# Kernel optimization log

Hardware: AMD Instinct MI355X
Metric: run time of the kernel (lower is better)

The kernel has to match this reference:

```python
import jax, jax.numpy as jnp
import numpy as np

E = 8          # num_experts
K = 2          # num_experts_per_tok
NORM_TOPK = True
B, S, D, F = 2, 1024, 2048, 1024  # batch, seq, hidden, moe_intermediate


def _kaiming_uniform(key, shape):
    # moe_fused_kaiming_uniform_: bound = sqrt(3*5 / in_features), in_features = shape[-1]
    bound = float(np.sqrt(3.0 * 5.0 / shape[-1]))
    return jax.random.uniform(key, shape, jnp.float32, -bound, bound)


def setup_inputs() -> dict:
    key = jax.random.key(0)
    k0, k1, k2, k3, k4 = jax.random.split(key, 5)
    gate_bound = float(1.0 / np.sqrt(D))  # nn.Linear default init
    return {
        "hidden_states": jax.random.normal(k0, (B, S, D), jnp.float32),
        "gate_w": jax.random.uniform(k1, (E, D), jnp.float32, -gate_bound, gate_bound),
        "w_gate_proj": _kaiming_uniform(k2, (E, F, D)),
        "w_up_proj": _kaiming_uniform(k3, (E, F, D)),
        "w_down_proj": _kaiming_uniform(k4, (E, D, F)),
    }


def reference(hidden_states, gate_w, w_gate_proj, w_up_proj, w_down_proj):
    b, s, d = hidden_states.shape
    x = hidden_states.reshape(-1, d)                      # [T, D]
    T = x.shape[0]

    # Router: softmax in fp32, top-k, optional renorm
    router_logits = x @ gate_w.T                          # [T, E]
    probs = jax.nn.softmax(router_logits.astype(jnp.float32), axis=-1)
    routing_weights, selected = jax.lax.top_k(probs, K)   # [T, K], [T, K]
    if NORM_TOPK:
        routing_weights = routing_weights / routing_weights.sum(-1, keepdims=True)
    routing_weights = routing_weights.astype(x.dtype)

    # Dense combine weights: c[t, e] = sum_k rw[t,k] * (sel[t,k]==e)
    combine = jnp.zeros((T, E), x.dtype).at[jnp.arange(T)[:, None], selected].add(routing_weights)

    # Expert SwiGLU FFN (dense over experts; combine zeros out unrouted experts,
    # identical math to sorted grouped-GEMM dispatch in the original)
    g = jnp.einsum('td,efd->tef', x, w_gate_proj)         # [T, E, F]
    u = jnp.einsum('td,efd->tef', x, w_up_proj)           # [T, E, F]
    h = jax.nn.silu(g) * u                                # [T, E, F]
    out = jnp.einsum('tef,edf,te->td', h, w_down_proj, combine)  # [T, D]

    return out.reshape(b, s, d), router_logits
```

## Files before the change

### kernel.cpp

```cpp
#include <hip/hip_runtime.h>
#include <stdint.h>

#define T_TOK 2048
#define DIM   2048
#define FDIM  1024
#define NE    8
#define MAXTILES 40

typedef __attribute__((ext_vector_type(8))) short short8;
typedef __attribute__((ext_vector_type(4))) float f32x4;

__device__ __forceinline__ unsigned short f2b(float f) {
  union { float f; unsigned int i; } x; x.f = f;
  unsigned int r = x.i + 0x7fffu + ((x.i >> 16) & 1u);
  return (unsigned short)(r >> 16);
}

__device__ __forceinline__ void async16(void* lds, const void* g) {
  __builtin_amdgcn_global_load_lds(
      (const __attribute__((address_space(1))) void*)g,
      (__attribute__((address_space(3))) void*)lds, 16, 0, 0);
}

__global__ __launch_bounds__(256) void cvt_x_k(const float* __restrict__ x,
                                               unsigned short* __restrict__ xb)
{
  int i = (blockIdx.x * 256 + threadIdx.x) * 8;
  float4 a = *(const float4*)(x + i);
  float4 b = *(const float4*)(x + i + 4);
  ushort4 o0, o1;
  o0.x = f2b(a.x); o0.y = f2b(a.y); o0.z = f2b(a.z); o0.w = f2b(a.w);
  o1.x = f2b(b.x); o1.y = f2b(b.y); o1.z = f2b(b.z); o1.w = f2b(b.w);
  *(ushort4*)(xb + i) = o0;
  *(ushort4*)(xb + i + 4) = o1;
}

__global__ __launch_bounds__(256) void router_k(
    const float* __restrict__ x, const float* __restrict__ gw,
    float* __restrict__ topkw, int* __restrict__ topke, int* __restrict__ counts,
    float* __restrict__ logits_out)
{
  int wave = threadIdx.x >> 6, lane = threadIdx.x & 63;
  int t = blockIdx.x * 4 + wave;
  const float* xr = x + (size_t)t * DIM;
  float acc[NE];
#pragma unroll
  for (int e = 0; e < NE; e++) acc[e] = 0.f;
  for (int d = lane * 4; d < DIM; d += 256) {
    float4 xv = *(const float4*)(xr + d);
#pragma unroll
    for (int e = 0; e < NE; e++) {
      float4 gv = *(const float4*)(gw + e * DIM + d);
      acc[e] += xv.x * gv.x + xv.y * gv.y + xv.z * gv.z + xv.w * gv.w;
    }
  }
#pragma unroll
  for (int off = 32; off > 0; off >>= 1) {
#pragma unroll
    for (int e = 0; e < NE; e++) acc[e] += __shfl_down(acc[e], off);
  }
  if (lane == 0) {
    float m = acc[0];
#pragma unroll
    for (int e = 1; e < NE; e++) m = fmaxf(m, acc[e]);
    float p[NE];
#pragma unroll
    for (int e = 0; e < NE; e++) p[e] = __expf(acc[e] - m);
    int e0 = 0;
#pragma unroll
    for (int e = 1; e < NE; e++) if (acc[e] > acc[e0]) e0 = e;
    int e1 = -1;
#pragma unroll
    for (int e = 0; e < NE; e++) if (e != e0 && (e1 < 0 || acc[e] > acc[e1])) e1 = e;
    float s = p[e0] + p[e1];
    topkw[t * 2] = p[e0] / s;
    topkw[t * 2 + 1] = p[e1] / s;
    topke[t * 2] = e0; topke[t * 2 + 1] = e1;
    atomicAdd(&counts[e0], 1);
    atomicAdd(&counts[e1], 1);
#pragma unroll
    for (int e = 0; e < NE; e++) logits_out[t * NE + e] = acc[e];
  }
}

__global__ void scan_k(const int* __restrict__ counts, int* __restrict__ offsets,
                       int* __restrict__ cursors, int4* __restrict__ tiles,
                       int* __restrict__ ntiles)
{
  if (threadIdx.x == 0 && blockIdx.x == 0) {
    int o = 0, nt = 0;
    for (int e = 0; e < NE; e++) {
      offsets[e] = o; cursors[e] = o;
      int c = counts[e];
      for (int r = 0; r < c; r += 128) {
        int rows = c - r < 128 ? c - r : 128;
        tiles[nt] = make_int4(e, o + r, rows, 0);
        nt++;
      }
      o += c;
    }
    offsets[NE] = o;
    *ntiles = nt;
  }
}

__global__ void scatter_k(const int* __restrict__ topke, int* __restrict__ cursors,
                          int* __restrict__ perm)
{
  int i = blockIdx.x * blockDim.x + threadIdx.x;
  int e = topke[i];
  int s = atomicAdd(&cursors[e], 1);
  perm[s] = i;
}

__global__ __launch_bounds__(256) void gemm1_k(
    const unsigned short* __restrict__ xb,
    const float* __restrict__ wg,
    const float* __restrict__ wu,
    const int* __restrict__ perm, const float* __restrict__ topkw,
    const int4* __restrict__ tiles, const int* __restrict__ ntiles,
    unsigned short* __restrict__ H)
{
  __shared__ short As[128 * 32];
  __shared__ short Bgs[64 * 32];
  __shared__ short Bus[64 * 32];
  __shared__ int rowtok[128];
  __shared__ float roww[128];

  if (blockIdx.x >= *ntiles) return;
  int4 tm = tiles[blockIdx.x];
  int e = tm.x, row0 = tm.y, nrows = tm.z;
  int tid = threadIdx.x;
  if (tid < 128) {
    int r = tid < nrows ? tid : (nrows - 1);
    int pid = perm[row0 + r];
    rowtok[tid] = pid >> 1;
    roww[tid] = topkw[pid];
  }
  __syncthreads();

  int f0 = blockIdx.y * 64;
  int crow = tid >> 2;
  int ccol = (tid & 3) * 8;
  const unsigned short* a0 = xb + (size_t)rowtok[crow] * DIM + ccol;
  const unsigned short* a1 = xb + (size_t)rowtok[crow + 64] * DIM + ccol;
  const float* bg32 = wg + ((size_t)e * FDIM + f0 + crow) * DIM + ccol;
  const float* bu32 = wu + ((size_t)e * FDIM + f0 + crow) * DIM + ccol;
  short* as0 = As + tid * 8;
  short* as1 = As + (256 + tid) * 8;

  int wave = tid >> 6, lane = tid & 63;
  int wm = wave >> 1, wn = wave & 1;
  int lrow = lane & 15, quad = lane >> 4;

  f32x4 accg[4][2], accu[4][2];
#pragma unroll
  for (int i = 0; i < 4; i++)
#pragma unroll
    for (int j = 0; j < 2; j++) {
      accg[i][j] = (f32x4){0.f, 0.f, 0.f, 0.f};
      accu[i][j] = (f32x4){0.f, 0.f, 0.f, 0.f};
    }

  const short* arp = As + (wm * 64 + lrow) * 32 + quad * 8;
  const short* bgp = Bgs + (wn * 32 + lrow) * 32 + quad * 8;
  const short* bup = Bus + (wn * 32 + lrow) * 32 + quad * 8;

#pragma unroll 1
  for (int k0 = 0; k0 < DIM; k0 += 32) {
    async16(as0, a0 + k0);
    async16(as1, a1 + k0);
    float4 g0 = *(const float4*)(bg32 + k0);
    float4 g1 = *(const float4*)(bg32 + k0 + 4);
    float4 u0 = *(const float4*)(bu32 + k0);
    float4 u1 = *(const float4*)(bu32 + k0 + 4);
    short8 gs, us;
    gs[0] = f2b(g0.x); gs[1] = f2b(g0.y); gs[2] = f2b(g0.z); gs[3] = f2b(g0.w);
    gs[4] = f2b(g1.x); gs[5] = f2b(g1.y); gs[6] = f2b(g1.z); gs[7] = f2b(g1.w);
    us[0] = f2b(u0.x); us[1] = f2b(u0.y); us[2] = f2b(u0.z); us[3] = f2b(u0.w);
    us[4] = f2b(u1.x); us[5] = f2b(u1.y); us[6] = f2b(u1.z); us[7] = f2b(u1.w);
    *(short8*)(Bgs + tid * 8) = gs;
    *(short8*)(Bus + tid * 8) = us;
    __syncthreads();
    short8 af[4], bgf[2], buf2[2];
#pragma unroll
    for (int i = 0; i < 4; i++) af[i] = *(const short8*)(arp + i * 16 * 32);
#pragma unroll
    for (int j = 0; j < 2; j++) {
      bgf[j]  = *(const short8*)(bgp + j * 16 * 32);
      buf2[j] = *(const short8*)(bup + j * 16 * 32);
    }
#pragma unroll
    for (int i = 0; i < 4; i++)
#pragma unroll
      for (int j = 0; j < 2; j++) {
        accg[i][j] = __builtin_amdgcn_mfma_f32_16x16x32_bf16(af[i], bgf[j], accg[i][j], 0, 0, 0);
        accu[i][j] = __builtin_amdgcn_mfma_f32_16x16x32_bf16(af[i], buf2[j], accu[i][j], 0, 0, 0);
      }
    __syncthreads();
  }

#pragma unroll
  for (int i = 0; i < 4; i++) {
#pragma unroll
    for (int reg = 0; reg < 4; reg++) {
      int r = wm * 64 + i * 16 + quad * 4 + reg;
      if (r < nrows) {
        float w = roww[r];
#pragma unroll
        for (int j = 0; j < 2; j++) {
          float g = accg[i][j][reg], u = accu[i][j][reg];
          float h = g * u * w / (1.f + __expf(-g));
          H[(size_t)(row0 + r) * FDIM + f0 + wn * 32 + j * 16 + lrow] = f2b(h);
        }
      }
    }
  }
}

__global__ __launch_bounds__(256) void gemm2_k(
    const unsigned short* __restrict__ H,
    const float* __restrict__ wd,
    const int* __restrict__ perm,
    const int4* __restrict__ tiles, const int* __restrict__ ntiles,
    float* __restrict__ out)
{
  __shared__ short Hs[128 * 32];
  __shared__ short Bs[64 * 32];
  __shared__ int rowtok[128];

  if (blockIdx.x >= *ntiles) return;
  int4 tm = tiles[blockIdx.x];
  int e = tm.x, row0 = tm.y, nrows = tm.z;
  int tid = threadIdx.x;
  if (tid < 128) {
    int r = tid < nrows ? tid : (nrows - 1);
    rowtok[tid] = perm[row0 + r] >> 1;
  }
  __syncthreads();

  int d0 = blockIdx.y * 64;
  int crow = tid >> 2, ccol = (tid & 3) * 8;
  const unsigned short* a0 = H + (size_t)(row0 + crow) * FDIM + ccol;
  const unsigned short* a1 = H + (size_t)(row0 + crow + 64) * FDIM + ccol;
  const float* b32 = wd + ((size_t)e * DIM + d0 + crow) * FDIM + ccol;
  short* hs0 = Hs + tid * 8;
  short* hs1 = Hs + (256 + tid) * 8;

  int wave = tid >> 6, lane = tid & 63;
  int wm = wave >> 1, wn = wave & 1;
  int lrow = lane & 15, quad = lane >> 4;

  f32x4 acc[4][2];
#pragma unroll
  for (int i = 0; i < 4; i++)
#pragma unroll
    for (int j = 0; j < 2; j++) acc[i][j] = (f32x4){0.f, 0.f, 0.f, 0.f};

  const short* arp = Hs + (wm * 64 + lrow) * 32 + quad * 8;
  const short* brp = Bs + (wn * 32 + lrow) * 32 + quad * 8;

#pragma unroll 1
  for (int k0 = 0; k0 < FDIM; k0 += 32) {
    async16(hs0, a0 + k0);
    async16(hs1, a1 + k0);
    float4 b0 = *(const float4*)(b32 + k0);
    float4 b1 = *(const float4*)(b32 + k0 + 4);
    short8 bsv;
    bsv[0] = f2b(b0.x); bsv[1] = f2b(b0.y); bsv[2] = f2b(b0.z); bsv[3] = f2b(b0.w);
    bsv[4] = f2b(b1.x); bsv[5] = f2b(b1.y); bsv[6] = f2b(b1.z); bsv[7] = f2b(b1.w);
    *(short8*)(Bs + tid * 8) = bsv;
    __syncthreads();
    short8 af[4], bf[2];
#pragma unroll
    for (int i = 0; i < 4; i++) af[i] = *(const short8*)(arp + i * 16 * 32);
#pragma unroll
    for (int j = 0; j < 2; j++) bf[j] = *(const short8*)(brp + j * 16 * 32);
#pragma unroll
    for (int i = 0; i < 4; i++)
#pragma unroll
      for (int j = 0; j < 2; j++)
        acc[i][j] = __builtin_amdgcn_mfma_f32_16x16x32_bf16(af[i], bf[j], acc[i][j], 0, 0, 0);
    __syncthreads();
  }

#pragma unroll
  for (int i = 0; i < 4; i++) {
#pragma unroll
    for (int reg = 0; reg < 4; reg++) {
      int r = wm * 64 + i * 16 + quad * 4 + reg;
      if (r < nrows) {
        int t = rowtok[r];
#pragma unroll
        for (int j = 0; j < 2; j++) {
          atomicAdd(&out[(size_t)t * DIM + d0 + wn * 32 + j * 16 + lrow], acc[i][j][reg]);
        }
      }
    }
  }
}

extern "C" void kernel_launch(void* const* d_in, const int* in_sizes, int n_in,
                              void* d_out, int out_size, void* d_ws, size_t ws_size,
                              hipStream_t stream)
{
  const float* x  = (const float*)d_in[0];
  const float* gw = (const float*)d_in[1];
  const float* wg = (const float*)d_in[2];
  const float* wu = (const float*)d_in[3];
  const float* wd = (const float*)d_in[4];
  float* out = (float*)d_out;
  float* logits_out = out + (size_t)T_TOK * DIM;

  char* ws = (char*)d_ws;
  float* topkw   = (float*)(ws + 0);
  int*   topke   = (int*)(ws + 16384);
  int*   counts  = (int*)(ws + 32768);
  int*   offsets = (int*)(ws + 32768 + 64);
  int*   cursors = (int*)(ws + 32768 + 128);
  int*   ntiles  = (int*)(ws + 32768 + 192);
  int4*  tiles   = (int4*)(ws + 32768 + 256);
  int*   perm    = (int*)(ws + 32768 + 2048);
  unsigned short* xb = (unsigned short*)(ws + (1 << 16));
  unsigned short* H  = (unsigned short*)(ws + (12u << 20));

  hipMemsetAsync(d_out, 0, (size_t)out_size * sizeof(float), stream);
  hipMemsetAsync(counts, 0, 64, stream);

  cvt_x_k<<<(T_TOK * DIM) / 2048, 256, 0, stream>>>(x, xb);
  router_k<<<T_TOK / 4, 256, 0, stream>>>(x, gw, topkw, topke, counts, logits_out);
  scan_k<<<1, 64, 0, stream>>>(counts, offsets, cursors, tiles, ntiles);
  scatter_k<<<(T_TOK * 2) / 256, 256, 0, stream>>>(topke, cursors, perm);
  gemm1_k<<<dim3(MAXTILES, FDIM / 64), 256, 0, stream>>>(xb, wg, wu, perm, topkw, tiles, ntiles, H);
  gemm2_k<<<dim3(MAXTILES, DIM / 64), 256, 0, stream>>>(H, wd, perm, tiles, ntiles, out);
}
```

Before: 437.3 us.

## Pre-convert expert weights to bf16 and use async-LDS bf16 grouped GEMMs

```diff
diff --git a/kernel.cpp b/kernel.cpp
--- a/kernel.cpp
+++ b/kernel.cpp
@@ -22,32 +22,36 @@
       (__attribute__((address_space(3))) void*)lds, 16, 0, 0);
 }
 
-__global__ __launch_bounds__(256) void cvt_x_k(const float* __restrict__ x,
-                                               unsigned short* __restrict__ xb)
-{
-  int i = (blockIdx.x * 256 + threadIdx.x) * 8;
-  float4 a = *(const float4*)(x + i);
-  float4 b = *(const float4*)(x + i + 4);
+__global__ __launch_bounds__(256) void cvt_w_k(const float* __restrict__ src,
+                                               unsigned short* __restrict__ dst)
+{
+  size_t i = ((size_t)blockIdx.x * 256 + threadIdx.x) * 8;
+  float4 a = *(const float4*)(src + i);
+  float4 b = *(const float4*)(src + i + 4);
   ushort4 o0, o1;
   o0.x = f2b(a.x); o0.y = f2b(a.y); o0.z = f2b(a.z); o0.w = f2b(a.w);
   o1.x = f2b(b.x); o1.y = f2b(b.y); o1.z = f2b(b.z); o1.w = f2b(b.w);
-  *(ushort4*)(xb + i) = o0;
-  *(ushort4*)(xb + i + 4) = o1;
+  *(ushort4*)(dst + i) = o0;
+  *(ushort4*)(dst + i + 4) = o1;
 }
 
 __global__ __launch_bounds__(256) void router_k(
     const float* __restrict__ x, const float* __restrict__ gw,
     float* __restrict__ topkw, int* __restrict__ topke, int* __restrict__ counts,
-    float* __restrict__ logits_out)
+    float* __restrict__ logits_out, unsigned short* __restrict__ xb)
 {
   int wave = threadIdx.x >> 6, lane = threadIdx.x & 63;
   int t = blockIdx.x * 4 + wave;
   const float* xr = x + (size_t)t * DIM;
+  unsigned short* xbr = xb + (size_t)t * DIM;
   float acc[NE];
 #pragma unroll
   for (int e = 0; e < NE; e++) acc[e] = 0.f;
   for (int d = lane * 4; d < DIM; d += 256) {
     float4 xv = *(const float4*)(xr + d);
+    ushort4 xo;
+    xo.x = f2b(xv.x); xo.y = f2b(xv.y); xo.z = f2b(xv.z); xo.w = f2b(xv.w);
+    *(ushort4*)(xbr + d) = xo;
 #pragma unroll
     for (int e = 0; e < NE; e++) {
       float4 gv = *(const float4*)(gw + e * DIM + d);
@@ -113,7 +117,188 @@
   perm[s] = i;
 }
 
-__global__ __launch_bounds__(256) void gemm1_k(
+
+__global__ __launch_bounds__(256) void gemm1_bf_k(
+    const unsigned short* __restrict__ xb,
+    const unsigned short* __restrict__ wgb,
+    const unsigned short* __restrict__ wub,
+    const int* __restrict__ perm, const float* __restrict__ topkw,
+    const int4* __restrict__ tiles, const int* __restrict__ ntiles,
+    unsigned short* __restrict__ H)
+{
+  __shared__ short As[128 * 32];
+  __shared__ short Bgs[64 * 32];
+  __shared__ short Bus[64 * 32];
+  __shared__ int rowtok[128];
+  __shared__ float roww[128];
+
+  if (blockIdx.x >= *ntiles) return;
+  int4 tm = tiles[blockIdx.x];
+  int e = tm.x, row0 = tm.y, nrows = tm.z;
+  int tid = threadIdx.x;
+  if (tid < 128) {
+    int r = tid < nrows ? tid : (nrows - 1);
+    int pid = perm[row0 + r];
+    rowtok[tid] = pid >> 1;
+    roww[tid] = topkw[pid];
+  }
+  __syncthreads();
+
+  int f0 = blockIdx.y * 64;
+  int crow = tid >> 2;
+  int ccol = (tid & 3) * 8;
+  const unsigned short* a0 = xb + (size_t)rowtok[crow] * DIM + ccol;
+  const unsigned short* a1 = xb + (size_t)rowtok[crow + 64] * DIM + ccol;
+  const unsigned short* bg = wgb + ((size_t)e * FDIM + f0 + crow) * DIM + ccol;
+  const unsigned short* bu = wub + ((size_t)e * FDIM + f0 + crow) * DIM + ccol;
+  short* as0 = As + tid * 8;
+  short* as1 = As + (256 + tid) * 8;
+  short* bgs = Bgs + tid * 8;
+  short* bus = Bus + tid * 8;
+
+  int wave = tid >> 6, lane = tid & 63;
+  int wm = wave >> 1, wn = wave & 1;
+  int lrow = lane & 15, quad = lane >> 4;
+
+  f32x4 accg[4][2], accu[4][2];
+#pragma unroll
+  for (int i = 0; i < 4; i++)
+#pragma unroll
+    for (int j = 0; j < 2; j++) {
+      accg[i][j] = (f32x4){0.f, 0.f, 0.f, 0.f};
+      accu[i][j] = (f32x4){0.f, 0.f, 0.f, 0.f};
+    }
+
+  const short* arp = As + (wm * 64 + lrow) * 32 + quad * 8;
+  const short* bgp = Bgs + (wn * 32 + lrow) * 32 + quad * 8;
+  const short* bup = Bus + (wn * 32 + lrow) * 32 + quad * 8;
+
+#pragma unroll 1
+  for (int k0 = 0; k0 < DIM; k0 += 32) {
+    async16(as0, a0 + k0);
+    async16(as1, a1 + k0);
+    async16(bgs, bg + k0);
+    async16(bus, bu + k0);
+    __syncthreads();
+    short8 af[4], bgf[2], buf2[2];
+#pragma unroll
+    for (int i = 0; i < 4; i++) af[i] = *(const short8*)(arp + i * 16 * 32);
+#pragma unroll
+    for (int j = 0; j < 2; j++) {
+      bgf[j]  = *(const short8*)(bgp + j * 16 * 32);
+      buf2[j] = *(const short8*)(bup + j * 16 * 32);
+    }
+#pragma unroll
+    for (int i = 0; i < 4; i++)
+#pragma unroll
+      for (int j = 0; j < 2; j++) {
+        accg[i][j] = __builtin_amdgcn_mfma_f32_16x16x32_bf16(af[i], bgf[j], accg[i][j], 0, 0, 0);
+        accu[i][j] = __builtin_amdgcn_mfma_f32_16x16x32_bf16(af[i], buf2[j], accu[i][j], 0, 0, 0);
+      }
+    __syncthreads();
+  }
+
+#pragma unroll
+  for (int i = 0; i < 4; i++) {
+#pragma unroll
+    for (int reg = 0; reg < 4; reg++) {
+      int r = wm * 64 + i * 16 + quad * 4 + reg;
+      if (r < nrows) {
+        float w = roww[r];
+#pragma unroll
+        for (int j = 0; j < 2; j++) {
+          float g = accg[i][j][reg], u = accu[i][j][reg];
+          float h = g * u * w / (1.f + __expf(-g));
+          H[(size_t)(row0 + r) * FDIM + f0 + wn * 32 + j * 16 + lrow] = f2b(h);
+        }
+      }
+    }
+  }
+}
+
+__global__ __launch_bounds__(256) void gemm2_bf_k(
+    const unsigned short* __restrict__ H,
+    const unsigned short* __restrict__ wdb,
+    const int* __restrict__ perm,
+    const int4* __restrict__ tiles, const int* __restrict__ ntiles,
+    float* __restrict__ out)
+{
+  __shared__ short Hs[128 * 32];
+  __shared__ short Bs[128 * 32];
+  __shared__ int rowtok[128];
+
+  if (blockIdx.x >= *ntiles) return;
+  int4 tm = tiles[blockIdx.x];
+  int e = tm.x, row0 = tm.y, nrows = tm.z;
+  int tid = threadIdx.x;
+  if (tid < 128) {
+    int r = tid < nrows ? tid : (nrows - 1);
+    rowtok[tid] = perm[row0 + r] >> 1;
+  }
+  __syncthreads();
+
+  int d0 = blockIdx.y * 128;
+  int crow = tid >> 2, ccol = (tid & 3) * 8;
+  const unsigned short* a0 = H + (size_t)(row0 + crow) * FDIM + ccol;
+  const unsigned short* a1 = H + (size_t)(row0 + crow + 64) * FDIM + ccol;
+  const unsigned short* b0 = wdb + ((size_t)e * DIM + d0 + crow) * FDIM + ccol;
+  const unsigned short* b1 = b0 + (size_t)64 * FDIM;
+  short* hs0 = Hs + tid * 8;
+  short* hs1 = Hs + (256 + tid) * 8;
+  short* bs0 = Bs + tid * 8;
+  short* bs1 = Bs + (256 + tid) * 8;
+
+  int wave = tid >> 6, lane = tid & 63;
+  int wm = wave >> 1, wn = wave & 1;
+  int lrow = lane & 15, quad = lane >> 4;
+
+  f32x4 acc[4][4];
+#pragma unroll
+  for (int i = 0; i < 4; i++)
+#pragma unroll
+    for (int j = 0; j < 4; j++) acc[i][j] = (f32x4){0.f, 0.f, 0.f, 0.f};
+
+  const short* arp = Hs + (wm * 64 + lrow) * 32 + quad * 8;
+  const short* brp = Bs + (wn * 64 + lrow) * 32 + quad * 8;
+
+#pragma unroll 1
+  for (int k0 = 0; k0 < FDIM; k0 += 32) {
+    async16(hs0, a0 + k0);
+    async16(hs1, a1 + k0);
+    async16(bs0, b0 + k0);
+    async16(bs1, b1 + k0);
+    __syncthreads();
+    short8 af[4], bf[4];
+#pragma unroll
+    for (int i = 0; i < 4; i++) af[i] = *(const short8*)(arp + i * 16 * 32);
+#pragma unroll
+    for (int j = 0; j < 4; j++) bf[j] = *(const short8*)(brp + j * 16 * 32);
+#pragma unroll
+    for (int i = 0; i < 4; i++)
+#pragma unroll
+      for (int j = 0; j < 4; j++)
+        acc[i][j] = __builtin_amdgcn_mfma_f32_16x16x32_bf16(af[i], bf[j], acc[i][j], 0, 0, 0);
+    __syncthreads();
+  }
+
+#pragma unroll
+  for (int i = 0; i < 4; i++) {
+#pragma unroll
+    for (int reg = 0; reg < 4; reg++) {
+      int r = wm * 64 + i * 16 + quad * 4 + reg;
+      if (r < nrows) {
+        int t = rowtok[r];
+#pragma unroll
+        for (int j = 0; j < 4; j++) {
+          atomicAdd(&out[(size_t)t * DIM + d0 + wn * 64 + j * 16 + lrow], acc[i][j][reg]);
+        }
+      }
+    }
+  }
+}
+
+
+__global__ __launch_bounds__(256) void gemm1_f32_k(
     const unsigned short* __restrict__ xb,
     const float* __restrict__ wg,
     const float* __restrict__ wu,
@@ -218,7 +403,7 @@
   }
 }
 
-__global__ __launch_bounds__(256) void gemm2_k(
+__global__ __launch_bounds__(256) void gemm2_f32_k(
     const unsigned short* __restrict__ H,
     const float* __restrict__ wd,
     const int* __restrict__ perm,
@@ -321,16 +506,29 @@
   int*   ntiles  = (int*)(ws + 32768 + 192);
   int4*  tiles   = (int4*)(ws + 32768 + 256);
   int*   perm    = (int*)(ws + 32768 + 2048);
-  unsigned short* xb = (unsigned short*)(ws + (1 << 16));
-  unsigned short* H  = (unsigned short*)(ws + (12u << 20));
+  unsigned short* xb  = (unsigned short*)(ws + (1u << 16));
+  unsigned short* H   = (unsigned short*)(ws + (9u  << 20));
+  unsigned short* wgb = (unsigned short*)(ws + (18u << 20));
+  unsigned short* wub = (unsigned short*)(ws + (50u << 20));
+  unsigned short* wdb = wgb;
+  const size_t WS_NEED = (size_t)82u << 20;
 
   hipMemsetAsync(d_out, 0, (size_t)out_size * sizeof(float), stream);
   hipMemsetAsync(counts, 0, 64, stream);
 
-  cvt_x_k<<<(T_TOK * DIM) / 2048, 256, 0, stream>>>(x, xb);
-  router_k<<<T_TOK / 4, 256, 0, stream>>>(x, gw, topkw, topke, counts, logits_out);
+  router_k<<<T_TOK / 4, 256, 0, stream>>>(x, gw, topkw, topke, counts, logits_out, xb);
   scan_k<<<1, 64, 0, stream>>>(counts, offsets, cursors, tiles, ntiles);
   scatter_k<<<(T_TOK * 2) / 256, 256, 0, stream>>>(topke, cursors, perm);
-  gemm1_k<<<dim3(MAXTILES, FDIM / 64), 256, 0, stream>>>(xb, wg, wu, perm, topkw, tiles, ntiles, H);
-  gemm2_k<<<dim3(MAXTILES, DIM / 64), 256, 0, stream>>>(H, wd, perm, tiles, ntiles, out);
-}
+
+  if (ws_size >= WS_NEED) {
+    const int nblk = (NE * FDIM * DIM) / 2048;
+    cvt_w_k<<<nblk, 256, 0, stream>>>(wg, wgb);
+    cvt_w_k<<<nblk, 256, 0, stream>>>(wu, wub);
+    gemm1_bf_k<<<dim3(MAXTILES, FDIM / 64), 256, 0, stream>>>(xb, wgb, wub, perm, topkw, tiles, ntiles, H);
+    cvt_w_k<<<nblk, 256, 0, stream>>>(wd, wdb);
+    gemm2_bf_k<<<dim3(MAXTILES, DIM / 128), 256, 0, stream>>>(H, wdb, perm, tiles, ntiles, out);
+  } else {
+    gemm1_f32_k<<<dim3(MAXTILES, FDIM / 64), 256, 0, stream>>>(xb, wg, wu, perm, topkw, tiles, ntiles, H);
+    gemm2_f32_k<<<dim3(MAXTILES, DIM / 64), 256, 0, stream>>>(H, wd, perm, tiles, ntiles, out);
+  }
+}
```

Measured after the change: 418.4 us. 4.3% less time.
